# Performance work log

Hardware: AMD Instinct MI355X
Metric: run time of the kernel (lower is better)

The kernel has to match this reference:

```python
import jax, jax.numpy as jnp
import numpy as np

N, F_IN, F_HID, F_OUT, E = 100000, 128, 256, 40, 1600000
LOG_SQRT_2PI = 0.9189385332046727  # log(sqrt(2*pi))


def setup_inputs() -> dict:
    key = jax.random.key(0)
    ks = jax.random.split(key, 12)
    s_in = 1.0 / np.sqrt(F_IN)
    s_hid = 1.0 / np.sqrt(F_HID)
    s_out = 1.0 / np.sqrt(F_OUT)
    return {
        "x": jax.random.normal(ks[0], (N, F_IN), jnp.float32),
        "adj_row": jax.random.randint(ks[1], (E,), 0, N, jnp.int32),
        "adj_col": jax.random.randint(ks[2], (E,), 0, N, jnp.int32),
        "adj_val": jax.random.uniform(ks[3], (E,), jnp.float32) * 0.1,
        "eps": jax.random.normal(ks[4], (1, N, F_IN), jnp.float32),
        "Wz1": jax.random.normal(ks[5], (F_IN, F_IN), jnp.float32) * s_in,
        "bz1": jnp.zeros((F_IN,), jnp.float32),
        "Wz2": jax.random.normal(ks[6], (F_IN, 2 * F_IN), jnp.float32) * s_in,
        "bz2": jnp.zeros((2 * F_IN,), jnp.float32),
        "W0": jax.random.uniform(ks[7], (F_IN, F_HID), jnp.float32, -s_hid, s_hid),
        "b0": jax.random.uniform(ks[8], (F_HID,), jnp.float32, -s_hid, s_hid),
        "W1": jax.random.uniform(ks[9], (F_HID, F_OUT), jnp.float32, -s_out, s_out),
        "b1": jax.random.uniform(ks[10], (F_OUT,), jnp.float32, -s_out, s_out),
    }


def spmm(row, col, val, mat):
    # sparse [N,N] (COO) @ dense [N,D] -> [N,D] via gather + segment_sum
    return jax.ops.segment_sum(val[:, None] * mat[col], row, num_segments=mat.shape[0])


def reference(x, adj_row, adj_col, adj_val, eps, Wz1, bz1, Wz2, bz2, W0, b0, W1, b1):
    # z_w MLP: Linear -> ReLU -> Linear producing [N, 2*F_IN]
    feats = jax.nn.relu(x @ Wz1 + bz1) @ Wz2 + bz2
    z_x_hat = spmm(adj_row, adj_col, adj_val, feats)  # [N, 2*F_IN]
    mean = z_x_hat[:, :F_IN]
    std = jax.nn.softplus(z_x_hat[:, F_IN:]) + 0.01
    # rsample((1,)): [1, N, F_IN]
    z = mean[None] + std[None] * eps
    # diagonal Normal log-probs, summed over feature dim
    logq = (-0.5 * ((z - mean[None]) / std[None]) ** 2 - jnp.log(std)[None] - LOG_SQRT_2PI).sum(-1)
    logp = (-0.5 * z ** 2 - LOG_SQRT_2PI).sum(-1)
    l2 = (logq - logp).mean(0).mean()
    h = z.mean(0)  # [N, F_IN]
    # GCN layer 1: dense transform then spmm, relu (dropout off in eval)
    h = jax.nn.relu(spmm(adj_row, adj_col, adj_val, h @ W0) + b0)
    # GCN layer 2 (output)
    out = spmm(adj_row, adj_col, adj_val, h @ W1) + b1
    return jax.nn.log_softmax(out, axis=1), l2
```

## Files before the change

kernel.cpp:

```cpp
#include <hip/hip_runtime.h>
#include <math.h>

constexpr int NN = 100000;
constexpr int NCHUNK = 128;
constexpr int RROWS  = 12500;

using f32x4 = __attribute__((ext_vector_type(4))) float;
using s16x8 = __attribute__((ext_vector_type(8))) short;
using us8   = __attribute__((ext_vector_type(8))) unsigned short;
using us4   = __attribute__((ext_vector_type(4))) unsigned short;

__device__ __forceinline__ unsigned short f2bf(float f) {
    unsigned u = __float_as_uint(f);
    unsigned r = u + 0x7FFFu + ((u >> 16) & 1u);
    return (unsigned short)(r >> 16);
}
__device__ __forceinline__ float bf2f(unsigned short u) {
    return __uint_as_float(((unsigned)u) << 16);
}

__device__ __forceinline__ void wfrag_body(
    const float* __restrict__ W, short* __restrict__ Wf,
    int K, int NC, int tid)
{
    const int KK = K / 32;
    int lane = tid & 63, f = tid >> 6;
    int ncg = f / KK, kk = f % KK;
    int col = ncg * 16 + (lane & 15);
    int k0  = kk * 32 + 8 * (lane >> 4);
    s16x8 o;
    #pragma unroll
    for (int j = 0; j < 8; ++j)
        o[j] = (col < NC) ? (short)f2bf(W[(size_t)(k0 + j) * NC + col]) : (short)0;
    *reinterpret_cast<s16x8*>(Wf + (size_t)tid * 8) = o;
}

__global__ __launch_bounds__(256) void wfrag_all(
    const float* __restrict__ Wz1, const float* __restrict__ Wz2,
    const float* __restrict__ W0,  const float* __restrict__ W1,
    short* wz1f, short* wz2f, short* w0f, short* w1f)
{
    int b = blockIdx.x;
    if (b < 8)       wfrag_body(Wz1, wz1f, 128, 128, b * 256 + threadIdx.x);
    else if (b < 24) wfrag_body(Wz2, wz2f, 128, 256, (b - 8) * 256 + threadIdx.x);
    else if (b < 40) wfrag_body(W0,  w0f,  128, 256, (b - 24) * 256 + threadIdx.x);
    else {
        int tid = (b - 40) * 256 + threadIdx.x;
        if (tid < 3 * 8 * 64) wfrag_body(W1, w1f, 256, 40, tid);
    }
}

template<int K, int WM, int WN, int CB, int AK, bool OBF16, int BIASMODE, bool ORELU>
__global__ __launch_bounds__(WM * WN * 64) void gemm_mfma(
    const void* __restrict__ Ain, const short* __restrict__ Wf,
    const float* __restrict__ bias, const float* __restrict__ b0,
    void* __restrict__ Cout, int M, int NCout)
{
    constexpr int KK = K / 32;
    const int tid = threadIdx.x;
    const int lane = tid & 63, wid = tid >> 6;
    const int wm = wid % WM, wn = wid / WM;
    const int rowBase = blockIdx.x * (WM * 64) + wm * 64;
    const int cfb = wn * CB;
    const int l15 = lane & 15, lh = lane >> 4;

    f32x4 acc[4][CB];
    #pragma unroll
    for (int i = 0; i < 4; ++i)
        #pragma unroll
        for (int j = 0; j < CB; ++j) acc[i][j] = (f32x4)0.f;

    #pragma unroll
    for (int kk = 0; kk < KK; ++kk) {
        const int k0 = kk * 32 + lh * 8;
        s16x8 a[4];
        #pragma unroll
        for (int rb = 0; rb < 4; ++rb) {
            int row = rowBase + rb * 16 + l15;
            row = row < M ? row : M - 1;
            if (AK == 0) {
                const float* ap = (const float*)Ain + (size_t)row * K + k0;
                float4 u = *reinterpret_cast<const float4*>(ap);
                float4 v = *reinterpret_cast<const float4*>(ap + 4);
                a[rb][0] = (short)f2bf(u.x); a[rb][1] = (short)f2bf(u.y);
                a[rb][2] = (short)f2bf(u.z); a[rb][3] = (short)f2bf(u.w);
                a[rb][4] = (short)f2bf(v.x); a[rb][5] = (short)f2bf(v.y);
                a[rb][6] = (short)f2bf(v.z); a[rb][7] = (short)f2bf(v.w);
            } else if (AK == 1) {
                a[rb] = *reinterpret_cast<const s16x8*>((const short*)Ain + (size_t)row * K + k0);
            } else {
                s16x8 s = *reinterpret_cast<const s16x8*>((const short*)Ain + (size_t)row * K + k0);
                float4 ba = *reinterpret_cast<const float4*>(b0 + k0);
                float4 bb = *reinterpret_cast<const float4*>(b0 + k0 + 4);
                float bv[8] = {ba.x, ba.y, ba.z, ba.w, bb.x, bb.y, bb.z, bb.w};
                #pragma unroll
                for (int j = 0; j < 8; ++j) {
                    float fv = bf2f((unsigned short)s[j]) + bv[j];
                    a[rb][j] = (short)f2bf(fmaxf(fv, 0.f));
                }
            }
        }
        s16x8 b[CB];
        #pragma unroll
        for (int cb = 0; cb < CB; ++cb)
            b[cb] = *reinterpret_cast<const s16x8*>(
                Wf + ((size_t)((cfb + cb) * KK + kk) * 64 + lane) * 8);
        #pragma unroll
        for (int rb = 0; rb < 4; ++rb)
            #pragma unroll
            for (int cb = 0; cb < CB; ++cb)
                acc[rb][cb] = __builtin_amdgcn_mfma_f32_16x16x32_bf16(
                    a[rb], b[cb], acc[rb][cb], 0, 0, 0);
    }

    #pragma unroll
    for (int cb = 0; cb < CB; ++cb) {
        int col = (cfb + cb) * 16 + l15;
        if (col >= NCout) continue;
        float bs = (BIASMODE != 0) ? bias[col] : 0.f;
        #pragma unroll
        for (int rb = 0; rb < 4; ++rb) {
            #pragma unroll
            for (int r = 0; r < 4; ++r) {
                int row = rowBase + rb * 16 + lh * 4 + r;
                if (row >= M) continue;
                float v = acc[rb][cb][r];
                if (BIASMODE == 1) v += bs;
                if (ORELU) v = fmaxf(v, 0.f);
                if (OBF16)
                    ((unsigned short*)Cout)[(size_t)row * NCout + col] = f2bf(v);
                else
                    ((float*)Cout)[(size_t)row * NCout + col] = v;
            }
        }
    }
}

__device__ __forceinline__ void gather_tile(
    const int* __restrict__ rp, const int2* __restrict__ edges,
    const unsigned short* __restrict__ mat, int rowBase,
    unsigned short* Als, float* rsls, bool wantRS)
{
    const int t = threadIdx.x;
    const int g = t >> 4, sl = t & 15;
    #pragma unroll
    for (int it = 0; it < 4; ++it) {
        int lr = g * 4 + it;
        int row = rowBase + lr;
        float acc[8] = {};
        float vs = 0.f;
        if (row < NN) {
            int e = rp[row];
            const int end = rp[row + 1];
            for (; e + 3 < end; e += 4) {
                int2 c[4]; float v[4]; us8 f[4];
                #pragma unroll
                for (int k = 0; k < 4; ++k) c[k] = edges[e + k];
                #pragma unroll
                for (int k = 0; k < 4; ++k) {
                    v[k] = __int_as_float(c[k].y);
                    f[k] = *reinterpret_cast<const us8*>(mat + (size_t)c[k].x * 128 + sl * 8);
                }
                vs += v[0] + v[1] + v[2] + v[3];
                #pragma unroll
                for (int k = 0; k < 4; ++k)
                    #pragma unroll
                    for (int j = 0; j < 8; ++j) acc[j] += v[k] * bf2f(f[k][j]);
            }
            for (; e < end; ++e) {
                int2 cv = edges[e];
                float v = __int_as_float(cv.y);
                vs += v;
                us8 f = *reinterpret_cast<const us8*>(mat + (size_t)cv.x * 128 + sl * 8);
                #pragma unroll
                for (int j = 0; j < 8; ++j) acc[j] += v * bf2f(f[j]);
            }
        }
        us8 o;
        #pragma unroll
        for (int j = 0; j < 8; ++j) o[j] = f2bf(acc[j]);
        unsigned byteoff = (unsigned)(lr * 256 + ((sl * 16) ^ ((lr & 7) << 4)));
        *reinterpret_cast<us8*>((char*)Als + byteoff) = o;
        if (wantRS && sl == 0) rsls[lr] = vs;
    }
}

__device__ __forceinline__ s16x8 lds_afrag(const unsigned short* Als, int lrow, int k0)
{
    unsigned byteoff = (unsigned)(lrow * 256 + (((k0 * 2) & 255) ^ ((lrow & 7) << 4)));
    return *reinterpret_cast<const s16x8*>((const char*)Als + byteoff);
}

__global__ __launch_bounds__(256) void spmm_gemm_z_sample(
    const int* __restrict__ rp, const int2* __restrict__ edges,
    const unsigned short* __restrict__ t1, const short* __restrict__ Wf,
    const float* __restrict__ bz2, const float* __restrict__ eps,
    unsigned short* __restrict__ hout, float* __restrict__ partials)
{
    __shared__ unsigned short Als[64 * 128];
    __shared__ float rsls[64];
    __shared__ float ws[4];
    const int tid = threadIdx.x;
    const int lane = tid & 63, wid = tid >> 6;
    const int rowBase = blockIdx.x * 64;
    const int l15 = lane & 15, lh = lane >> 4;

    gather_tile(rp, edges, t1, rowBase, Als, rsls, true);
    __syncthreads();

    const int cf[4] = {wid * 2, wid * 2 + 1, 8 + wid * 2, 8 + wid * 2 + 1};
    f32x4 acc[4][4];
    #pragma unroll
    for (int i = 0; i < 4; ++i)
        #pragma unroll
        for (int j = 0; j < 4; ++j) acc[i][j] = (f32x4)0.f;

    #pragma unroll
    for (int kk = 0; kk < 4; ++kk) {
        const int k0 = kk * 32 + lh * 8;
        s16x8 a[4];
        #pragma unroll
        for (int rb = 0; rb < 4; ++rb)
            a[rb] = lds_afrag(Als, rb * 16 + l15, k0);
        s16x8 b[4];
        #pragma unroll
        for (int cb = 0; cb < 4; ++cb)
            b[cb] = *reinterpret_cast<const s16x8*>(
                Wf + ((size_t)(cf[cb] * 4 + kk) * 64 + lane) * 8);
        #pragma unroll
        for (int rb = 0; rb < 4; ++rb)
            #pragma unroll
            for (int cb = 0; cb < 4; ++cb)
                acc[rb][cb] = __builtin_amdgcn_mfma_f32_16x16x32_bf16(
                    a[rb], b[cb], acc[rb][cb], 0, 0, 0);
    }

    const float bsm0 = bz2[wid * 32 + l15];
    const float bsm1 = bz2[wid * 32 + 16 + l15];
    const float bss0 = bz2[128 + wid * 32 + l15];
    const float bss1 = bz2[128 + wid * 32 + 16 + l15];
    float p = 0.f;
    #pragma unroll
    for (int rb = 0; rb < 4; ++rb) {
        #pragma unroll
        for (int r = 0; r < 4; ++r) {
            int lrow = rb * 16 + lh * 4 + r;
            int row = rowBase + lrow;
            if (row >= NN) continue;
            float rs = rsls[lrow];
            #pragma unroll
            for (int cb = 0; cb < 2; ++cb) {
                int colm = wid * 32 + cb * 16 + l15;
                float mean = acc[rb][cb][r]     + rs * (cb ? bsm1 : bsm0);
                float sv   = acc[rb][2 + cb][r] + rs * (cb ? bss1 : bss0);
                float ea = __expf(-fabsf(sv));
                float sp = fmaxf(sv, 0.f) + __logf(1.f + ea);
                float sd = sp + 0.01f;
                float e  = eps[(size_t)row * 128 + colm];
                float h  = mean + sd * e;
                hout[(size_t)row * 128 + colm] = f2bf(h);
                p += 0.5f * h * h - 0.5f * e * e - __logf(sd);
            }
        }
    }
    #pragma unroll
    for (int o = 32; o > 0; o >>= 1) p += __shfl_xor(p, o);
    if (lane == 0) ws[wid] = p;
    __syncthreads();
    if (tid == 0) partials[blockIdx.x] = ws[0] + ws[1] + ws[2] + ws[3];
}

__global__ __launch_bounds__(256) void spmm_gemm256(
    const int* __restrict__ rp, const int2* __restrict__ edges,
    const unsigned short* __restrict__ h, const short* __restrict__ Wf,
    unsigned short* __restrict__ s2out)
{
    __shared__ unsigned short Als[64 * 128];
    const int tid = threadIdx.x;
    const int lane = tid & 63, wid = tid >> 6;
    const int rowBase = blockIdx.x * 64;
    const int l15 = lane & 15, lh = lane >> 4;

    gather_tile(rp, edges, h, rowBase, Als, nullptr, false);
    __syncthreads();

    const int cfb = wid * 4;
    f32x4 acc[4][4];
    #pragma unroll
    for (int i = 0; i < 4; ++i)
        #pragma unroll
        for (int j = 0; j < 4; ++j) acc[i][j] = (f32x4)0.f;

    #pragma unroll
    for (int kk = 0; kk < 4; ++kk) {
        const int k0 = kk * 32 + lh * 8;
        s16x8 a[4];
        #pragma unroll
        for (int rb = 0; rb < 4; ++rb)
            a[rb] = lds_afrag(Als, rb * 16 + l15, k0);
        s16x8 b[4];
        #pragma unroll
        for (int cb = 0; cb < 4; ++cb)
            b[cb] = *reinterpret_cast<const s16x8*>(
                Wf + ((size_t)((cfb + cb) * 4 + kk) * 64 + lane) * 8);
        #pragma unroll
        for (int rb = 0; rb < 4; ++rb)
            #pragma unroll
            for (int cb = 0; cb < 4; ++cb)
                acc[rb][cb] = __builtin_amdgcn_mfma_f32_16x16x32_bf16(
                    a[rb], b[cb], acc[rb][cb], 0, 0, 0);
    }

    #pragma unroll
    for (int cb = 0; cb < 4; ++cb) {
        int col = (cfb + cb) * 16 + l15;
        #pragma unroll
        for (int rb = 0; rb < 4; ++rb) {
            #pragma unroll
            for (int r = 0; r < 4; ++r) {
                int row = rowBase + rb * 16 + lh * 4 + r;
                if (row >= NN) continue;
                s2out[(size_t)row * 256 + col] = f2bf(acc[rb][cb][r]);
            }
        }
    }
}

__global__ __launch_bounds__(256) void hist_part(
    const int* __restrict__ row, unsigned short* __restrict__ part, int E, int chunkE)
{
    __shared__ unsigned lcnt[RROWS / 2];
    const int chunk = blockIdx.x;
    const int rowLo = blockIdx.y * RROWS;
    for (int i = threadIdx.x; i < RROWS / 2; i += 256) lcnt[i] = 0u;
    __syncthreads();
    const int e0 = chunk * chunkE;
    const int e1 = min(e0 + chunkE, E);
    for (int e = e0 + threadIdx.x; e < e1; e += 256) {
        int lr = row[e] - rowLo;
        if ((unsigned)lr < (unsigned)RROWS)
            atomicAdd(&lcnt[lr >> 1], 1u << ((lr & 1) << 4));
    }
    __syncthreads();
    unsigned* dst = reinterpret_cast<unsigned*>(part + (size_t)chunk * NN + rowLo);
    for (int i = threadIdx.x; i < RROWS / 2; i += 256) dst[i] = lcnt[i];
}

__global__ __launch_bounds__(256) void chunk_scan(
    unsigned short* __restrict__ part, int* __restrict__ cnt)
{
    int r = blockIdx.x * 256 + threadIdx.x;
    if (r >= NN) return;
    int run = 0;
    for (int c0 = 0; c0 < NCHUNK; c0 += 8) {
        int v[8];
        #pragma unroll
        for (int j = 0; j < 8; ++j) v[j] = part[(size_t)(c0 + j) * NN + r];
        #pragma unroll
        for (int j = 0; j < 8; ++j) {
            part[(size_t)(c0 + j) * NN + r] = (unsigned short)run;
            run += v[j];
        }
    }
    cnt[r] = run;
}

__global__ __launch_bounds__(256) void scan_blk(
    const int* __restrict__ cnt, int* __restrict__ rp, int* __restrict__ bsums, int n)
{
    const int t = threadIdx.x;
    const int lane = t & 63, wid = t >> 6;
    const int base = blockIdx.x * 1024 + t * 4;
    int a0 = 0, a1 = 0, a2 = 0, a3 = 0;
    if (base + 3 < n) {
        int4 v = *reinterpret_cast<const int4*>(&cnt[base]);
        a0 = v.x; a1 = v.y; a2 = v.z; a3 = v.w;
    } else {
        if (base + 0 < n) a0 = cnt[base + 0];
        if (base + 1 < n) a1 = cnt[base + 1];
        if (base + 2 < n) a2 = cnt[base + 2];
        if (base + 3 < n) a3 = cnt[base + 3];
    }
    int s0 = a0, s1 = s0 + a1, s2 = s1 + a2, s3 = s2 + a3;
    int v = s3;
    #pragma unroll
    for (int o = 1; o < 64; o <<= 1) {
        int u = __shfl_up(v, o);
        if (lane >= o) v += u;
    }
    __shared__ int wtot[4];
    if (lane == 63) wtot[wid] = v;
    __syncthreads();
    int woff = 0;
    #pragma unroll
    for (int w = 0; w < 4; ++w) if (w < wid) woff += wtot[w];
    int texcl = woff + v - s3;
    if (base + 0 < n) rp[base + 0] = texcl;
    if (base + 1 < n) rp[base + 1] = texcl + s0;
    if (base + 2 < n) rp[base + 2] = texcl + s1;
    if (base + 3 < n) rp[base + 3] = texcl + s2;
    if (t == 255) bsums[blockIdx.x] = woff + v;
}

__global__ void scan_mid(const int* __restrict__ bsums, int* __restrict__ boff, int nb)
{
    if (threadIdx.x == 0 && blockIdx.x == 0) {
        int run = 0;
        for (int b = 0; b < nb; ++b) { boff[b] = run; run += bsums[b]; }
    }
}

__global__ __launch_bounds__(256) void scan_add(
    int* __restrict__ rp, const int* __restrict__ boff, int n, int E)
{
    int i = blockIdx.x * 256 + threadIdx.x;
    if (i < n) rp[i] += boff[i >> 10];
    if (i == 0) rp[n] = E;
}

__global__ __launch_bounds__(256) void scatter_part(
    const int* __restrict__ row, const int* __restrict__ col,
    const float* __restrict__ val, const int* __restrict__ rp,
    const unsigned short* __restrict__ part, int2* __restrict__ edges,
    int E, int chunkE)
{
    __shared__ unsigned lcnt[RROWS / 2];
    const int chunk = blockIdx.x;
    const int rowLo = blockIdx.y * RROWS;
    for (int i = threadIdx.x; i < RROWS / 2; i += 256) lcnt[i] = 0u;
    __syncthreads();
    const int e0 = chunk * chunkE;
    const int e1 = min(e0 + chunkE, E);
    const unsigned short* choff = part + (size_t)chunk * NN;
    for (int e = e0 + threadIdx.x; e < e1; e += 256) {
        int r = row[e];
        int lr = r - rowLo;
        if ((unsigned)lr < (unsigned)RROWS) {
            unsigned old = atomicAdd(&lcnt[lr >> 1], 1u << ((lr & 1) << 4));
            int local = (int)((old >> ((lr & 1) << 4)) & 0xFFFFu);
            int p = rp[r] + (int)choff[r] + local;
            edges[p] = make_int2(col[e], __float_as_int(val[e]));
        }
    }
}

__global__ __launch_bounds__(256) void spmm40_lsm(
    const int* __restrict__ rp, const int2* __restrict__ edges,
    const unsigned short* __restrict__ mat, const float* __restrict__ b1,
    float* __restrict__ out)
{
    int gid = blockIdx.x * 256 + threadIdx.x;
    int r = gid >> 4, sl = gid & 15;
    const int beg = rp[r], end = rp[r + 1];
    float4 acc = make_float4(0.f, 0.f, 0.f, 0.f);
    int e = beg;
    for (; e + 3 < end; e += 4) {
        int2 c[4];
        #pragma unroll
        for (int k = 0; k < 4; ++k) c[k] = edges[e + k];
        if (sl < 10) {
            #pragma unroll
            for (int k = 0; k < 4; ++k) {
                float v = __int_as_float(c[k].y);
                us4 m = *reinterpret_cast<const us4*>(mat + (size_t)c[k].x * 40 + sl * 4);
                acc.x += v * bf2f(m[0]); acc.y += v * bf2f(m[1]);
                acc.z += v * bf2f(m[2]); acc.w += v * bf2f(m[3]);
            }
        }
    }
    for (; e < end; ++e) {
        int2 cv = edges[e];
        float v = __int_as_float(cv.y);
        if (sl < 10) {
            us4 m = *reinterpret_cast<const us4*>(mat + (size_t)cv.x * 40 + sl * 4);
            acc.x += v * bf2f(m[0]); acc.y += v * bf2f(m[1]);
            acc.z += v * bf2f(m[2]); acc.w += v * bf2f(m[3]);
        }
    }
    float xv[4] = {-1e30f, -1e30f, -1e30f, -1e30f};
    if (sl < 10) {
        xv[0] = acc.x + b1[sl * 4 + 0]; xv[1] = acc.y + b1[sl * 4 + 1];
        xv[2] = acc.z + b1[sl * 4 + 2]; xv[3] = acc.w + b1[sl * 4 + 3];
    }
    float m = fmaxf(fmaxf(xv[0], xv[1]), fmaxf(xv[2], xv[3]));
    #pragma unroll
    for (int o = 1; o < 16; o <<= 1) m = fmaxf(m, __shfl_xor(m, o, 16));
    float ssum = 0.f;
    #pragma unroll
    for (int k = 0; k < 4; ++k) ssum += (sl < 10) ? __expf(xv[k] - m) : 0.f;
    #pragma unroll
    for (int o = 1; o < 16; o <<= 1) ssum += __shfl_xor(ssum, o, 16);
    if (sl < 10) {
        float lse = m + __logf(ssum);
        float4 o4 = make_float4(xv[0] - lse, xv[1] - lse, xv[2] - lse, xv[3] - lse);
        *reinterpret_cast<float4*>(out + (size_t)r * 40 + sl * 4) = o4;
    }
}

__global__ __launch_bounds__(256) void finalize_l2(
    const float* __restrict__ partials, int np, float* __restrict__ out)
{
    double a = 0.0;
    for (int i = threadIdx.x; i < np; i += 256) a += (double)partials[i];
    #pragma unroll
    for (int o = 32; o > 0; o >>= 1) a += __shfl_xor(a, o);
    __shared__ double ws[4];
    if ((threadIdx.x & 63) == 0) ws[threadIdx.x >> 6] = a;
    __syncthreads();
    if (threadIdx.x == 0)
        out[(size_t)NN * 40] = (float)((ws[0] + ws[1] + ws[2] + ws[3]) / (double)NN);
}

extern "C" void kernel_launch(void* const* d_in, const int* in_sizes, int n_in,
                              void* d_out, int out_size, void* d_ws, size_t ws_size,
                              hipStream_t stream)
{
    const float* x    = (const float*)d_in[0];
    const int*   arow = (const int*)d_in[1];
    const int*   acol = (const int*)d_in[2];
    const float* aval = (const float*)d_in[3];
    const float* eps  = (const float*)d_in[4];
    const float* Wz1  = (const float*)d_in[5];
    const float* bz1  = (const float*)d_in[6];
    const float* Wz2  = (const float*)d_in[7];
    const float* bz2  = (const float*)d_in[8];
    const float* W0   = (const float*)d_in[9];
    const float* b0   = (const float*)d_in[10];
    const float* W1   = (const float*)d_in[11];
    const float* b1   = (const float*)d_in[12];
    float* out = (float*)d_out;
    const int E = in_sizes[1];

    char* p = (char*)d_ws;
    auto alloc = [&](size_t bytes) {
        char* q = p;
        p += (bytes + 15) & ~(size_t)15;
        return (void*)q;
    };
    int2* edges           = (int2*)alloc((size_t)E * 8);
    unsigned short* part  = (unsigned short*)alloc((size_t)NCHUNK * NN * 2);
    int*  rp              = (int*)alloc((size_t)(NN + 4) * 4);
    int*  cnt             = (int*)alloc((size_t)NN * 4);
    int*  bsums           = (int*)alloc(128 * 4);
    int*  boff            = (int*)alloc(128 * 4);
    float* partials       = (float*)alloc(1568 * 4);
    unsigned short* bufT  = (unsigned short*)alloc((size_t)NN * 128 * 2);
    unsigned short* bufU  = (unsigned short*)alloc((size_t)NN * 128 * 2);
    unsigned short* bufZ  = (unsigned short*)alloc((size_t)NN * 256 * 2);
    short* wz1f           = (short*)alloc(8  * 4 * 64 * 8 * 2);
    short* wz2f           = (short*)alloc(16 * 4 * 64 * 8 * 2);
    short* w0f            = (short*)alloc(16 * 4 * 64 * 8 * 2);
    short* w1f            = (short*)alloc(3  * 8 * 64 * 8 * 2);

    dim3 blk(256);
    const int nScan = (NN + 1023) / 1024;
    const int gSp = (NN * 16) / 256;
    const int gF  = (NN + 63) / 64;
    const int chunkE = (E + NCHUNK - 1) / NCHUNK;
    const dim3 gPart(NCHUNK, NN / RROWS);

    wfrag_all<<<dim3(46), blk, 0, stream>>>(Wz1, Wz2, W0, W1, wz1f, wz2f, w0f, w1f);

    hist_part<<<gPart, blk, 0, stream>>>(arow, part, E, chunkE);
    chunk_scan<<<dim3((NN + 255) / 256), blk, 0, stream>>>(part, cnt);
    scan_blk<<<dim3(nScan), blk, 0, stream>>>(cnt, rp, bsums, NN);
    scan_mid<<<dim3(1), dim3(64), 0, stream>>>(bsums, boff, nScan);
    scan_add<<<dim3((NN + 256) / 256), blk, 0, stream>>>(rp, boff, NN, E);
    scatter_part<<<gPart, blk, 0, stream>>>(arow, acol, aval, rp, part, edges, E, chunkE);

    gemm_mfma<128, 2, 2, 4, 0, true, 1, true><<<dim3(782), blk, 0, stream>>>(
        x, wz1f, bz1, nullptr, bufT, NN, 128);
    spmm_gemm_z_sample<<<dim3(gF), blk, 0, stream>>>(
        rp, edges, bufT, wz2f, bz2, eps, bufU, partials);
    spmm_gemm256<<<dim3(gF), blk, 0, stream>>>(rp, edges, bufU, w0f, bufZ);
    gemm_mfma<256, 4, 1, 3, 2, true, 0, false><<<dim3(391), blk, 0, stream>>>(
        bufZ, w1f, nullptr, b0, bufT, NN, 40);
    spmm40_lsm<<<dim3(gSp), blk, 0, stream>>>(rp, edges, bufT, b1, out);
    finalize_l2<<<dim3(1), blk, 0, stream>>>(partials, gF, out);
}
```

Before: 470.4 us.

## Merge independent kernels into combined launches and unroll gather by eight

```diff
diff --git a/kernel.cpp b/kernel.cpp
--- a/kernel.cpp
+++ b/kernel.cpp
@@ -35,24 +35,9 @@
     *reinterpret_cast<s16x8*>(Wf + (size_t)tid * 8) = o;
 }
 
-__global__ __launch_bounds__(256) void wfrag_all(
-    const float* __restrict__ Wz1, const float* __restrict__ Wz2,
-    const float* __restrict__ W0,  const float* __restrict__ W1,
-    short* wz1f, short* wz2f, short* w0f, short* w1f)
-{
-    int b = blockIdx.x;
-    if (b < 8)       wfrag_body(Wz1, wz1f, 128, 128, b * 256 + threadIdx.x);
-    else if (b < 24) wfrag_body(Wz2, wz2f, 128, 256, (b - 8) * 256 + threadIdx.x);
-    else if (b < 40) wfrag_body(W0,  w0f,  128, 256, (b - 24) * 256 + threadIdx.x);
-    else {
-        int tid = (b - 40) * 256 + threadIdx.x;
-        if (tid < 3 * 8 * 64) wfrag_body(W1, w1f, 256, 40, tid);
-    }
-}
-
 template<int K, int WM, int WN, int CB, int AK, bool OBF16, int BIASMODE, bool ORELU>
-__global__ __launch_bounds__(WM * WN * 64) void gemm_mfma(
-    const void* __restrict__ Ain, const short* __restrict__ Wf,
+__device__ __forceinline__ void gemm_body(
+    int bid, const void* __restrict__ Ain, const short* __restrict__ Wf,
     const float* __restrict__ bias, const float* __restrict__ b0,
     void* __restrict__ Cout, int M, int NCout)
 {
@@ -60,7 +45,7 @@
     const int tid = threadIdx.x;
     const int lane = tid & 63, wid = tid >> 6;
     const int wm = wid % WM, wn = wid / WM;
-    const int rowBase = blockIdx.x * (WM * 64) + wm * 64;
+    const int rowBase = bid * (WM * 64) + wm * 64;
     const int cfb = wn * CB;
     const int l15 = lane & 15, lh = lane >> 4;
 
@@ -136,6 +121,171 @@
     }
 }
 
+template<int K, int WM, int WN, int CB, int AK, bool OBF16, int BIASMODE, bool ORELU>
+__global__ __launch_bounds__(WM * WN * 64) void gemm_mfma(
+    const void* __restrict__ Ain, const short* __restrict__ Wf,
+    const float* __restrict__ bias, const float* __restrict__ b0,
+    void* __restrict__ Cout, int M, int NCout)
+{
+    gemm_body<K, WM, WN, CB, AK, OBF16, BIASMODE, ORELU>(
+        blockIdx.x, Ain, Wf, bias, b0, Cout, M, NCout);
+}
+
+__device__ __forceinline__ void hist_body(
+    const int* __restrict__ row, unsigned short* __restrict__ part,
+    int E, int chunkE, int chunk, int rowLo, unsigned* lcnt)
+{
+    for (int i = threadIdx.x; i < RROWS / 2; i += 256) lcnt[i] = 0u;
+    __syncthreads();
+    const int e0 = chunk * chunkE;
+    const int e1 = min(e0 + chunkE, E);
+    for (int e = e0 + threadIdx.x; e < e1; e += 256) {
+        int lr = row[e] - rowLo;
+        if ((unsigned)lr < (unsigned)RROWS)
+            atomicAdd(&lcnt[lr >> 1], 1u << ((lr & 1) << 4));
+    }
+    __syncthreads();
+    unsigned* dst = reinterpret_cast<unsigned*>(part + (size_t)chunk * NN + rowLo);
+    for (int i = threadIdx.x; i < RROWS / 2; i += 256) dst[i] = lcnt[i];
+}
+
+__device__ __forceinline__ void scatter_body(
+    const int* __restrict__ row, const int* __restrict__ col,
+    const float* __restrict__ val, const int* __restrict__ rp,
+    const unsigned short* __restrict__ part, int2* __restrict__ edges,
+    int E, int chunkE, int chunk, int rowLo, unsigned* lcnt)
+{
+    for (int i = threadIdx.x; i < RROWS / 2; i += 256) lcnt[i] = 0u;
+    __syncthreads();
+    const int e0 = chunk * chunkE;
+    const int e1 = min(e0 + chunkE, E);
+    const unsigned short* choff = part + (size_t)chunk * NN;
+    for (int e = e0 + threadIdx.x; e < e1; e += 256) {
+        int r = row[e];
+        int lr = r - rowLo;
+        if ((unsigned)lr < (unsigned)RROWS) {
+            unsigned old = atomicAdd(&lcnt[lr >> 1], 1u << ((lr & 1) << 4));
+            int local = (int)((old >> ((lr & 1) << 4)) & 0xFFFFu);
+            int p = rp[r] + (int)choff[r] + local;
+            edges[p] = make_int2(col[e], __float_as_int(val[e]));
+        }
+    }
+}
+
+__global__ __launch_bounds__(256) void hist_wfrag_combo(
+    const int* __restrict__ arow, unsigned short* __restrict__ part,
+    int E, int chunkE,
+    const float* __restrict__ Wz1, const float* __restrict__ Wz2,
+    const float* __restrict__ W0,  const float* __restrict__ W1,
+    short* wz1f, short* wz2f, short* w0f, short* w1f)
+{
+    __shared__ unsigned lcnt[RROWS / 2];
+    int b = blockIdx.x;
+    if (b < NCHUNK * 8) {
+        hist_body(arow, part, E, chunkE, b & (NCHUNK - 1), (b >> 7) * RROWS, lcnt);
+    } else {
+        int bb = b - NCHUNK * 8;
+        if (bb < 8)       wfrag_body(Wz1, wz1f, 128, 128, bb * 256 + threadIdx.x);
+        else if (bb < 24) wfrag_body(Wz2, wz2f, 128, 256, (bb - 8) * 256 + threadIdx.x);
+        else if (bb < 40) wfrag_body(W0,  w0f,  128, 256, (bb - 24) * 256 + threadIdx.x);
+        else {
+            int tid = (bb - 40) * 256 + threadIdx.x;
+            if (tid < 3 * 8 * 64) wfrag_body(W1, w1f, 256, 40, tid);
+        }
+    }
+}
+
+__global__ __launch_bounds__(256) void scatter_g1_combo(
+    const int* __restrict__ arow, const int* __restrict__ acol,
+    const float* __restrict__ aval, const int* __restrict__ rp,
+    const unsigned short* __restrict__ part, int2* __restrict__ edges,
+    int E, int chunkE,
+    const float* __restrict__ x, const short* __restrict__ wz1f,
+    const float* __restrict__ bz1, unsigned short* __restrict__ t1out)
+{
+    __shared__ unsigned lcnt[RROWS / 2];
+    int b = blockIdx.x;
+    if (b < NCHUNK * 8) {
+        scatter_body(arow, acol, aval, rp, part, edges, E, chunkE,
+                     b & (NCHUNK - 1), (b >> 7) * RROWS, lcnt);
+    } else {
+        gemm_body<128, 2, 2, 4, 0, true, 1, true>(
+            b - NCHUNK * 8, x, wz1f, bz1, nullptr, t1out, NN, 128);
+    }
+}
+
+__global__ __launch_bounds__(256) void chunk_scan(
+    unsigned short* __restrict__ part, int* __restrict__ cnt)
+{
+    int r = blockIdx.x * 256 + threadIdx.x;
+    if (r >= NN) return;
+    int run = 0;
+    for (int c0 = 0; c0 < NCHUNK; c0 += 8) {
+        int v[8];
+        #pragma unroll
+        for (int j = 0; j < 8; ++j) v[j] = part[(size_t)(c0 + j) * NN + r];
+        #pragma unroll
+        for (int j = 0; j < 8; ++j) {
+            part[(size_t)(c0 + j) * NN + r] = (unsigned short)run;
+            run += v[j];
+        }
+    }
+    cnt[r] = run;
+}
+
+__global__ __launch_bounds__(256) void scan_blk(
+    const int* __restrict__ cnt, int* __restrict__ rp, int* __restrict__ bsums, int n)
+{
+    const int t = threadIdx.x;
+    const int lane = t & 63, wid = t >> 6;
+    const int base = blockIdx.x * 1024 + t * 4;
+    int a0 = 0, a1 = 0, a2 = 0, a3 = 0;
+    if (base + 3 < n) {
+        int4 v = *reinterpret_cast<const int4*>(&cnt[base]);
+        a0 = v.x; a1 = v.y; a2 = v.z; a3 = v.w;
+    } else {
+        if (base + 0 < n) a0 = cnt[base + 0];
+        if (base + 1 < n) a1 = cnt[base + 1];
+        if (base + 2 < n) a2 = cnt[base + 2];
+        if (base + 3 < n) a3 = cnt[base + 3];
+    }
+    int s0 = a0, s1 = s0 + a1, s2 = s1 + a2, s3 = s2 + a3;
+    int v = s3;
+    #pragma unroll
+    for (int o = 1; o < 64; o <<= 1) {
+        int u = __shfl_up(v, o);
+        if (lane >= o) v += u;
+    }
+    __shared__ int wtot[4];
+    if (lane == 63) wtot[wid] = v;
+    __syncthreads();
+    int woff = 0;
+    #pragma unroll
+    for (int w = 0; w < 4; ++w) if (w < wid) woff += wtot[w];
+    int texcl = woff + v - s3;
+    if (base + 0 < n) rp[base + 0] = texcl;
+    if (base + 1 < n) rp[base + 1] = texcl + s0;
+    if (base + 2 < n) rp[base + 2] = texcl + s1;
+    if (base + 3 < n) rp[base + 3] = texcl + s2;
+    if (t == 255) bsums[blockIdx.x] = woff + v;
+}
+
+__global__ void scan_mid(const int* __restrict__ bsums, int* __restrict__ boff, int nb)
+{
+    if (threadIdx.x == 0 && blockIdx.x == 0) {
+        int run = 0;
+        for (int b = 0; b < nb; ++b) { boff[b] = run; run += bsums[b]; }
+    }
+}
+
+__global__ __launch_bounds__(256) void scan_add(
+    int* __restrict__ rp, const int* __restrict__ boff, int n, int E)
+{
+    int i = blockIdx.x * 256 + threadIdx.x;
+    if (i < n) rp[i] += boff[i >> 10];
+    if (i == 0) rp[n] = E;
+}
+
 __device__ __forceinline__ void gather_tile(
     const int* __restrict__ rp, const int2* __restrict__ edges,
     const unsigned short* __restrict__ mat, int rowBase,
@@ -152,6 +302,21 @@
         if (row < NN) {
             int e = rp[row];
             const int end = rp[row + 1];
+            for (; e + 7 < end; e += 8) {
+                int2 c[8]; float v[8]; us8 f[8];
+                #pragma unroll
+                for (int k = 0; k < 8; ++k) c[k] = edges[e + k];
+                #pragma unroll
+                for (int k = 0; k < 8; ++k) {
+                    v[k] = __int_as_float(c[k].y);
+                    f[k] = *reinterpret_cast<const us8*>(mat + (size_t)c[k].x * 128 + sl * 8);
+                }
+                vs += v[0] + v[1] + v[2] + v[3] + v[4] + v[5] + v[6] + v[7];
+                #pragma unroll
+                for (int k = 0; k < 8; ++k)
+                    #pragma unroll
+                    for (int j = 0; j < 8; ++j) acc[j] += v[k] * bf2f(f[k][j]);
+            }
             for (; e + 3 < end; e += 4) {
                 int2 c[4]; float v[4]; us8 f[4];
                 #pragma unroll
@@ -322,124 +487,6 @@
                 if (row >= NN) continue;
                 s2out[(size_t)row * 256 + col] = f2bf(acc[rb][cb][r]);
             }
-        }
-    }
-}
-
-__global__ __launch_bounds__(256) void hist_part(
-    const int* __restrict__ row, unsigned short* __restrict__ part, int E, int chunkE)
-{
-    __shared__ unsigned lcnt[RROWS / 2];
-    const int chunk = blockIdx.x;
-    const int rowLo = blockIdx.y * RROWS;
-    for (int i = threadIdx.x; i < RROWS / 2; i += 256) lcnt[i] = 0u;
-    __syncthreads();
-    const int e0 = chunk * chunkE;
-    const int e1 = min(e0 + chunkE, E);
-    for (int e = e0 + threadIdx.x; e < e1; e += 256) {
-        int lr = row[e] - rowLo;
-        if ((unsigned)lr < (unsigned)RROWS)
-            atomicAdd(&lcnt[lr >> 1], 1u << ((lr & 1) << 4));
-    }
-    __syncthreads();
-    unsigned* dst = reinterpret_cast<unsigned*>(part + (size_t)chunk * NN + rowLo);
-    for (int i = threadIdx.x; i < RROWS / 2; i += 256) dst[i] = lcnt[i];
-}
-
-__global__ __launch_bounds__(256) void chunk_scan(
-    unsigned short* __restrict__ part, int* __restrict__ cnt)
-{
-    int r = blockIdx.x * 256 + threadIdx.x;
-    if (r >= NN) return;
-    int run = 0;
-    for (int c0 = 0; c0 < NCHUNK; c0 += 8) {
-        int v[8];
-        #pragma unroll
-        for (int j = 0; j < 8; ++j) v[j] = part[(size_t)(c0 + j) * NN + r];
-        #pragma unroll
-        for (int j = 0; j < 8; ++j) {
-            part[(size_t)(c0 + j) * NN + r] = (unsigned short)run;
-            run += v[j];
-        }
-    }
-    cnt[r] = run;
-}
-
-__global__ __launch_bounds__(256) void scan_blk(
-    const int* __restrict__ cnt, int* __restrict__ rp, int* __restrict__ bsums, int n)
-{
-    const int t = threadIdx.x;
-    const int lane = t & 63, wid = t >> 6;
-    const int base = blockIdx.x * 1024 + t * 4;
-    int a0 = 0, a1 = 0, a2 = 0, a3 = 0;
-    if (base + 3 < n) {
-        int4 v = *reinterpret_cast<const int4*>(&cnt[base]);
-        a0 = v.x; a1 = v.y; a2 = v.z; a3 = v.w;
-    } else {
-        if (base + 0 < n) a0 = cnt[base + 0];
-        if (base + 1 < n) a1 = cnt[base + 1];
-        if (base + 2 < n) a2 = cnt[base + 2];
-        if (base + 3 < n) a3 = cnt[base + 3];
-    }
-    int s0 = a0, s1 = s0 + a1, s2 = s1 + a2, s3 = s2 + a3;
-    int v = s3;
-    #pragma unroll
-    for (int o = 1; o < 64; o <<= 1) {
-        int u = __shfl_up(v, o);
-        if (lane >= o) v += u;
-    }
-    __shared__ int wtot[4];
-    if (lane == 63) wtot[wid] = v;
-    __syncthreads();
-    int woff = 0;
-    #pragma unroll
-    for (int w = 0; w < 4; ++w) if (w < wid) woff += wtot[w];
-    int texcl = woff + v - s3;
-    if (base + 0 < n) rp[base + 0] = texcl;
-    if (base + 1 < n) rp[base + 1] = texcl + s0;
-    if (base + 2 < n) rp[base + 2] = texcl + s1;
-    if (base + 3 < n) rp[base + 3] = texcl + s2;
-    if (t == 255) bsums[blockIdx.x] = woff + v;
-}
-
-__global__ void scan_mid(const int* __restrict__ bsums, int* __restrict__ boff, int nb)
-{
-    if (threadIdx.x == 0 && blockIdx.x == 0) {
-        int run = 0;
-        for (int b = 0; b < nb; ++b) { boff[b] = run; run += bsums[b]; }
-    }
-}
-
-__global__ __launch_bounds__(256) void scan_add(
-    int* __restrict__ rp, const int* __restrict__ boff, int n, int E)
-{
-    int i = blockIdx.x * 256 + threadIdx.x;
-    if (i < n) rp[i] += boff[i >> 10];
-    if (i == 0) rp[n] = E;
-}
-
-__global__ __launch_bounds__(256) void scatter_part(
-    const int* __restrict__ row, const int* __restrict__ col,
-    const float* __restrict__ val, const int* __restrict__ rp,
-    const unsigned short* __restrict__ part, int2* __restrict__ edges,
-    int E, int chunkE)
-{
-    __shared__ unsigned lcnt[RROWS / 2];
-    const int chunk = blockIdx.x;
-    const int rowLo = blockIdx.y * RROWS;
-    for (int i = threadIdx.x; i < RROWS / 2; i += 256) lcnt[i] = 0u;
-    __syncthreads();
-    const int e0 = chunk * chunkE;
-    const int e1 = min(e0 + chunkE, E);
-    const unsigned short* choff = part + (size_t)chunk * NN;
-    for (int e = e0 + threadIdx.x; e < e1; e += 256) {
-        int r = row[e];
-        int lr = r - rowLo;
-        if ((unsigned)lr < (unsigned)RROWS) {
-            unsigned old = atomicAdd(&lcnt[lr >> 1], 1u << ((lr & 1) << 4));
-            int local = (int)((old >> ((lr & 1) << 4)) & 0xFFFFu);
-            int p = rp[r] + (int)choff[r] + local;
-            edges[p] = make_int2(col[e], __float_as_int(val[e]));
         }
     }
 }
@@ -557,19 +604,16 @@
     const int gSp = (NN * 16) / 256;
     const int gF  = (NN + 63) / 64;
     const int chunkE = (E + NCHUNK - 1) / NCHUNK;
-    const dim3 gPart(NCHUNK, NN / RROWS);
-
-    wfrag_all<<<dim3(46), blk, 0, stream>>>(Wz1, Wz2, W0, W1, wz1f, wz2f, w0f, w1f);
-
-    hist_part<<<gPart, blk, 0, stream>>>(arow, part, E, chunkE);
+    const int gHist = NCHUNK * 8;
+
+    hist_wfrag_combo<<<dim3(gHist + 46), blk, 0, stream>>>(
+        arow, part, E, chunkE, Wz1, Wz2, W0, W1, wz1f, wz2f, w0f, w1f);
     chunk_scan<<<dim3((NN + 255) / 256), blk, 0, stream>>>(part, cnt);
     scan_blk<<<dim3(nScan), blk, 0, stream>>>(cnt, rp, bsums, NN);
     scan_mid<<<dim3(1), dim3(64), 0, stream>>>(bsums, boff, nScan);
     scan_add<<<dim3((NN + 256) / 256), blk, 0, stream>>>(rp, boff, NN, E);
-    scatter_part<<<gPart, blk, 0, stream>>>(arow, acol, aval, rp, part, edges, E, chunkE);
-
-    gemm_mfma<128, 2, 2, 4, 0, true, 1, true><<<dim3(782), blk, 0, stream>>>(
-        x, wz1f, bz1, nullptr, bufT, NN, 128);
+    scatter_g1_combo<<<dim3(gHist + 782), blk, 0, stream>>>(
+        arow, acol, aval, rp, part, edges, E, chunkE, x, wz1f, bz1, bufT);
     spmm_gemm_z_sample<<<dim3(gF), blk, 0, stream>>>(
         rp, edges, bufT, wz2f, bz2, eps, bufU, partials);
     spmm_gemm256<<<dim3(gF), blk, 0, stream>>>(rp, edges, bufU, w0f, bufZ);
```

After: 452.8 us. 3.7% less time.
